# Kernel optimization log

Hardware: AMD Instinct MI355X
Metric: run time of the kernel (lower is better)

Reference implementation:

```python
import jax, jax.numpy as jnp
import numpy as np
import math

DIM = 1024
H = 16
DH = DIM // H
B = 2
L = 1024


def setup_inputs() -> dict:
    key = jax.random.key(0)
    ks = jax.random.split(key, 8)
    s = 1.0 / math.sqrt(DIM)
    return {
        "Q": jax.random.normal(ks[0], (B, L, DIM), jnp.float32),
        "K": jax.random.normal(ks[1], (B, L, DIM), jnp.float32),
        "mask_Q": jax.random.bernoulli(ks[2], 0.1, (B, L)),
        "mask_K": jax.random.bernoulli(ks[3], 0.1, (B, L)),
        "Wq": jax.random.normal(ks[4], (DIM, DIM), jnp.float32) * s,
        "Wk": jax.random.normal(ks[5], (DIM, DIM), jnp.float32) * s,
        "Wv": jax.random.normal(ks[6], (DIM, DIM), jnp.float32) * s,
        "Wo": jax.random.normal(ks[7], (DIM, DIM), jnp.float32) * s,
    }


def reference(Q, K, mask_Q, mask_K, Wq, Wk, Wv, Wo):
    # V defaults to K. Masked positions of inputs are zeroed first.
    Qz = jnp.where(mask_Q[:, :, None], 0.0, Q)
    Kz = jnp.where(mask_K[:, :, None], 0.0, K)
    Vz = Kz  # V = K, masked with mask_K

    # Projections (nn.Linear, no bias): y = x @ W.T
    Qp = jnp.einsum('bld,ed->ble', Qz, Wq)
    Kp = jnp.einsum('bld,ed->ble', Kz, Wk)
    Vp = jnp.einsum('bld,ed->ble', Vz, Wv)

    # split heads: [B, L, H, DH] -> per-head attention
    qh = Qp.reshape(B, L, H, DH)
    kh = Kp.reshape(B, L, H, DH)
    vh = Vp.reshape(B, L, H, DH)

    # NOTE: original scales by sqrt(dim) (full dim), not sqrt(dim_split)
    scores = jnp.einsum('bqhd,bkhd->bhqk', qh, kh) / math.sqrt(DIM)

    # outer-product validity mask: valid iff both q and k positions unmasked
    valid = (~mask_Q)[:, None, :, None] & (~mask_K)[:, None, None, :]  # [B,1,Lq,Lk]
    A = jnp.where(valid, scores, -1e38)
    A = jax.nn.softmax(A, axis=-1)
    A = jnp.where(valid, A, 0.0)

    O = jnp.einsum('bhqk,bkhd->bqhd', A, vh).reshape(B, L, DIM)
    # residual uses the PROJECTED Q (Q was reassigned to fc_q(Q) in torch)
    O = Qp + O
    # masked_forward(fc_o, ...): fc_o applied, masked query rows forced to 0
    ff = jax.nn.relu(jnp.where(mask_Q[:, :, None], 0.0, jnp.einsum('bld,ed->ble', O, Wo)))
    O = O + ff
    return O
```

## Files before the change

### kernel.cpp

```cpp
#include <hip/hip_runtime.h>
#include <hip/hip_bf16.h>


#define DEV __device__ __forceinline__

typedef __attribute__((ext_vector_type(8))) short bf16x8;
typedef __attribute__((ext_vector_type(4))) float f32x4;
typedef __hip_bfloat16 bf16;

DEV void glds16(const bf16* g, bf16* s) {
  __builtin_amdgcn_global_load_lds(
      (const __attribute__((address_space(1))) void*)g,
      (__attribute__((address_space(3))) void*)s, 16, 0, 0);
}

DEV unsigned short f2bu(float x) {
  __hip_bfloat16 b = __float2bfloat16(x);
  unsigned short u;
  __builtin_memcpy(&u, &b, 2);
  return u;
}

__global__ void normalize_masks(const unsigned char* mq_raw, const unsigned char* mk_raw,
                                unsigned char* outq, unsigned char* outk,
                                unsigned long long* qm64, unsigned long long* km64) {
  __shared__ int cnt;
  int t = threadIdx.x;
  if (t == 0) cnt = 0;
  __syncthreads();
  int c = 0;
  for (int i = t; i < 2048; i += 256) c += (mq_raw[i] != 0);
  atomicAdd(&cnt, c);
  __syncthreads();
  bool isByte = cnt > 128;
  for (int i = t; i < 2048; i += 256) {
    unsigned char q, k;
    if (isByte) {
      q = (mq_raw[i] != 0); k = (mk_raw[i] != 0);
    } else {
      q = (((const int*)mq_raw)[i] != 0); k = (((const int*)mk_raw)[i] != 0);
    }
    outq[i] = q; outk[i] = k;
  }
  __syncthreads();
  if (t < 64) {
    const unsigned char* src = (t < 32) ? outk : outq;
    int idx = t & 31;
    unsigned long long m = 0;
    for (int j = 0; j < 64; ++j)
      m |= (unsigned long long)(src[idx * 64 + j] != 0) << j;
    if (t < 32) km64[idx] = m; else qm64[idx] = m;
  }
}

__global__ __launch_bounds__(256) void cast_qk(const float* __restrict__ Q,
                                               const float* __restrict__ K,
                                               const unsigned char* __restrict__ mq,
                                               const unsigned char* __restrict__ mk,
                                               bf16* __restrict__ oq, bf16* __restrict__ ok) {
  const float* X = blockIdx.z ? K : Q;
  const unsigned char* m = blockIdx.z ? mk : mq;
  bf16* out = blockIdx.z ? ok : oq;
  int i = (blockIdx.x * 256 + threadIdx.x) * 4;
  float4 v = *(const float4*)&X[i];
  if (m[i >> 10]) { v.x = 0.f; v.y = 0.f; v.z = 0.f; v.w = 0.f; }
  *(ushort4*)&out[i] = make_ushort4(f2bu(v.x), f2bu(v.y), f2bu(v.z), f2bu(v.w));
}

__global__ __launch_bounds__(256) void cast_w(const float* __restrict__ W0, const float* __restrict__ W1,
                                              const float* __restrict__ W2, const float* __restrict__ W3,
                                              bf16* __restrict__ o0, bf16* __restrict__ o1,
                                              bf16* __restrict__ o2, bf16* __restrict__ o3) {
  const float* X; bf16* out;
  switch (blockIdx.z) {
    case 0: X = W0; out = o0; break;
    case 1: X = W1; out = o1; break;
    case 2: X = W2; out = o2; break;
    default: X = W3; out = o3; break;
  }
  int i = (blockIdx.x * 256 + threadIdx.x) * 4;
  float4 v = *(const float4*)&X[i];
  *(ushort4*)&out[i] = make_ushort4(f2bu(v.x), f2bu(v.y), f2bu(v.z), f2bu(v.w));
}

template <typename EPI>
DEV void gemm128(const bf16* __restrict__ A, const bf16* __restrict__ W,
                 int K, int brow, int bcol, EPI&& epi) {
  __shared__ bf16 As[128 * 32];
  __shared__ bf16 Bs[128 * 32];
  const int t = threadIdx.x;
  const int l = t & 63;
  const int w = t >> 6;
  const int wr = w >> 1, wc = w & 1;

  const int rA0 = w * 32 + (l >> 2);
  const int kcol = (l & 3) * 8;

  f32x4 acc[4][4];
#pragma unroll
  for (int i = 0; i < 4; i++)
#pragma unroll
    for (int j = 0; j < 4; j++) acc[i][j] = (f32x4){0.f, 0.f, 0.f, 0.f};

  const int aoff = (wr * 64 + (l & 15)) * 32 + (l >> 4) * 8;
  const int boff = (wc * 64 + (l & 15)) * 32 + (l >> 4) * 8;

  for (int k0 = 0; k0 < K; k0 += 32) {
    __syncthreads();
#pragma unroll
    for (int c = 0; c < 2; ++c) {
      glds16(A + (size_t)(brow + rA0 + c * 16) * K + k0 + kcol, As + w * 1024 + c * 512);
      glds16(W + (size_t)(bcol + rA0 + c * 16) * K + k0 + kcol, Bs + w * 1024 + c * 512);
    }
    __syncthreads();

    bf16x8 a[4], b[4];
#pragma unroll
    for (int mi = 0; mi < 4; ++mi) a[mi] = *(const bf16x8*)&As[aoff + mi * 512];
#pragma unroll
    for (int ni = 0; ni < 4; ++ni) b[ni] = *(const bf16x8*)&Bs[boff + ni * 512];
#pragma unroll
    for (int mi = 0; mi < 4; ++mi)
#pragma unroll
      for (int ni = 0; ni < 4; ++ni)
        acc[mi][ni] = __builtin_amdgcn_mfma_f32_16x16x32_bf16(a[mi], b[ni], acc[mi][ni], 0, 0, 0);
  }

#pragma unroll
  for (int mi = 0; mi < 4; ++mi)
#pragma unroll
    for (int ni = 0; ni < 4; ++ni)
#pragma unroll
      for (int r = 0; r < 4; ++r) {
        int row = brow + wr * 64 + mi * 16 + (l >> 4) * 4 + r;
        int col = bcol + wc * 64 + ni * 16 + (l & 15);
        epi(row, col, acc[mi][ni][r]);
      }
}

__global__ __launch_bounds__(256) void proj_gemm(
    const bf16* __restrict__ Qz, const bf16* __restrict__ Kz,
    const bf16* __restrict__ Wq, const bf16* __restrict__ Wk, const bf16* __restrict__ Wv,
    float* __restrict__ Qpf, bf16* __restrict__ Qpb,
    bf16* __restrict__ Kpb, bf16* __restrict__ Vpb) {
  const int z = blockIdx.z;
  const int brow = blockIdx.x * 128, bcol = blockIdx.y * 128;
  if (z == 0) {
    gemm128(Qz, Wq, 1024, brow, bcol, [&](int row, int col, float v) {
      size_t idx = (size_t)row * 1024 + col;
      Qpf[idx] = v;
      Qpb[idx] = __float2bfloat16(v * 0.03125f);
    });
  } else if (z == 1) {
    gemm128(Kz, Wk, 1024, brow, bcol, [&](int row, int col, float v) {
      Kpb[(size_t)row * 1024 + col] = __float2bfloat16(v);
    });
  } else {
    gemm128(Kz, Wv, 1024, brow, bcol, [&](int row, int col, float v) {
      Vpb[(size_t)row * 1024 + col] = __float2bfloat16(v);
    });
  }
}

__global__ __launch_bounds__(256) void final_gemm(
    const bf16* __restrict__ Ob, const bf16* __restrict__ Wo,
    float* __restrict__ out, const unsigned char* __restrict__ mq) {
  const int brow = blockIdx.x * 128, bcol = blockIdx.y * 128;
  gemm128(Ob, Wo, 1024, brow, bcol, [&](int row, int col, float v) {
    size_t idx = (size_t)row * 1024 + col;
    float ff = mq[row] ? 0.f : fmaxf(v, 0.f);
    out[idx] = out[idx] + ff;
  });
}

__global__ __launch_bounds__(256) void attn_fused(
    const bf16* __restrict__ Qpb, const bf16* __restrict__ Kpb, const bf16* __restrict__ Vpb,
    const float* __restrict__ Qpf,
    const unsigned long long* __restrict__ qm64, const unsigned long long* __restrict__ km64,
    float* __restrict__ Of, bf16* __restrict__ Ob) {
  __shared__ bf16 Klds[64 * 64];
  __shared__ bf16 Vt[64 * 72];

  const int t = threadIdx.x, l = t & 63, w = t >> 6;
  const int q = l & 15, g = l >> 4;
  const int qt = blockIdx.x;
  const int b = blockIdx.y >> 4, h = blockIdx.y & 15;
  const size_t bbase = (size_t)b * 1024;

  const int qg = qt * 64 + w * 16 + q;
  const bf16* qptr = Qpb + (bbase + qg) * 1024 + h * 64 + g * 8;
  const bf16x8 qb0 = *(const bf16x8*)qptr;
  const bf16x8 qb1 = *(const bf16x8*)(qptr + 32);

  float mrun = -1e30f, srun = 0.f;
  f32x4 oacc[4];
#pragma unroll
  for (int mf = 0; mf < 4; ++mf) oacc[mf] = (f32x4){0.f, 0.f, 0.f, 0.f};

  const int krow_s = l >> 3;
  const int kcol_s = ((l & 7) ^ krow_s) * 8;

  const int vk0 = 2 * (t & 31);
  const int vdc = t >> 5;

  union { uint4 v; unsigned short s[8]; } u0, u1;
  {
    const bf16* g0 = Vpb + (bbase + vk0) * 1024 + h * 64 + vdc * 8;
    u0.v = *(const uint4*)g0;
    u1.v = *(const uint4*)(g0 + 1024);
  }

  for (int kt = 0; kt < 16; ++kt) {
    const int kbase = kt * 64;
    const unsigned long long km = km64[b * 16 + kt];
    const unsigned long long mloc = km >> (4 * g);

    __syncthreads();
#pragma unroll
    for (int j = 0; j < 8; ++j) {
      int d = vdc * 8 + j;
      unsigned int pk = (unsigned int)u0.s[j] | ((unsigned int)u1.s[j] << 16);
      *(unsigned int*)((char*)Vt + d * 144 + vk0 * 2) = pk;
    }
#pragma unroll
    for (int c = 0; c < 2; ++c) {
      int cw = w * 2 + c;
      glds16(Kpb + (bbase + kbase + cw * 8 + krow_s) * 1024 + h * 64 + kcol_s,
             Klds + cw * 512);
    }
    __syncthreads();

    if (kt < 15) {
      const bf16* g0 = Vpb + (bbase + kbase + 64 + vk0) * 1024 + h * 64 + vdc * 8;
      u0.v = *(const uint4*)g0;
      u1.v = *(const uint4*)(g0 + 1024);
    }

    f32x4 S[4];
#pragma unroll
    for (int mf = 0; mf < 4; ++mf) {
#pragma unroll
      for (int r = 0; r < 4; ++r)
        S[mf][r] = ((mloc >> (mf * 16 + r)) & 1ull) ? -1e30f : 0.f;
      const int row = mf * 16 + q;
      const int rowb = row * 128;
      const bf16x8 ka0 = *(const bf16x8*)((const char*)Klds + rowb + ((g ^ (row & 7)) * 16));
      const bf16x8 ka1 = *(const bf16x8*)((const char*)Klds + rowb + (((g + 4) ^ (row & 7)) * 16));
      S[mf] = __builtin_amdgcn_mfma_f32_16x16x32_bf16(ka0, qb0, S[mf], 0, 0, 0);
      S[mf] = __builtin_amdgcn_mfma_f32_16x16x32_bf16(ka1, qb1, S[mf], 0, 0, 0);
    }

    float vmax = -1e30f;
#pragma unroll
    for (int mf = 0; mf < 4; ++mf)
#pragma unroll
      for (int r = 0; r < 4; ++r) vmax = fmaxf(vmax, S[mf][r]);
    vmax = fmaxf(vmax, __shfl_xor(vmax, 16));
    vmax = fmaxf(vmax, __shfl_xor(vmax, 32));
    const float mnew = fmaxf(mrun, vmax);
    const float alpha = __expf(mrun - mnew);
    mrun = mnew;

    float psum = 0.f;
    unsigned int lo[4], hi[4];
#pragma unroll
    for (int mf = 0; mf < 4; ++mf) {
      float p0 = __expf(S[mf][0] - mnew), p1 = __expf(S[mf][1] - mnew);
      float p2 = __expf(S[mf][2] - mnew), p3 = __expf(S[mf][3] - mnew);
      psum += (p0 + p1) + (p2 + p3);
      lo[mf] = (unsigned int)f2bu(p0) | ((unsigned int)f2bu(p1) << 16);
      hi[mf] = (unsigned int)f2bu(p2) | ((unsigned int)f2bu(p3) << 16);
    }
    psum += __shfl_xor(psum, 16);
    psum += __shfl_xor(psum, 32);
    srun = srun * alpha + psum;
#pragma unroll
    for (int mf = 0; mf < 4; ++mf) oacc[mf] *= alpha;

    const int srcA = ((2 * g) & 3) * 16 + q;
    const int srcB = srcA + 16;
    const bool sel = (g >> 1) & 1;
#pragma unroll
    for (int ks = 0; ks < 2; ++ks) {
      unsigned int a0 = __shfl(lo[2 * ks], srcA), a1 = __shfl(hi[2 * ks], srcA);
      unsigned int a2 = __shfl(lo[2 * ks], srcB), a3 = __shfl(hi[2 * ks], srcB);
      unsigned int b0 = __shfl(lo[2 * ks + 1], srcA), b1 = __shfl(hi[2 * ks + 1], srcA);
      unsigned int b2 = __shfl(lo[2 * ks + 1], srcB), b3 = __shfl(hi[2 * ks + 1], srcB);
      uint4 pw;
      pw.x = sel ? b0 : a0; pw.y = sel ? b1 : a1;
      pw.z = sel ? b2 : a2; pw.w = sel ? b3 : a3;
      const bf16x8 pa = __builtin_bit_cast(bf16x8, pw);
#pragma unroll
      for (int mf = 0; mf < 4; ++mf) {
        const bf16x8 va = *(const bf16x8*)((const char*)Vt + (mf * 16 + q) * 144 + ks * 64 + g * 16);
        oacc[mf] = __builtin_amdgcn_mfma_f32_16x16x32_bf16(va, pa, oacc[mf], 0, 0, 0);
      }
    }
  }

  const unsigned long long qm = qm64[b * 16 + qt];
  const bool qvalid = !((qm >> (w * 16 + q)) & 1ull);
  const float inv = (qvalid && srun > 0.f) ? 1.f / srun : 0.f;
#pragma unroll
  for (int mf = 0; mf < 4; ++mf) {
    size_t idx = (bbase + qg) * 1024 + h * 64 + mf * 16 + g * 4;
    float4 qp = *(const float4*)&Qpf[idx];
    float4 val;
    val.x = qp.x + oacc[mf][0] * inv;
    val.y = qp.y + oacc[mf][1] * inv;
    val.z = qp.z + oacc[mf][2] * inv;
    val.w = qp.w + oacc[mf][3] * inv;
    *(float4*)&Of[idx] = val;
    *(ushort4*)&Ob[idx] = make_ushort4(f2bu(val.x), f2bu(val.y), f2bu(val.z), f2bu(val.w));
  }
}

extern "C" void kernel_launch(void* const* d_in, const int* in_sizes, int n_in,
                              void* d_out, int out_size, void* d_ws, size_t ws_size,
                              hipStream_t stream) {
  const float* Q = (const float*)d_in[0];
  const float* K = (const float*)d_in[1];
  const unsigned char* mQraw = (const unsigned char*)d_in[2];
  const unsigned char* mKraw = (const unsigned char*)d_in[3];
  const float* Wq = (const float*)d_in[4];
  const float* Wk = (const float*)d_in[5];
  const float* Wv = (const float*)d_in[6];
  const float* Wo = (const float*)d_in[7];
  float* out = (float*)d_out;

  char* ws = (char*)d_ws;
  const size_t MB = 1024 * 1024;
  bf16* Qz = (bf16*)(ws + 0);
  bf16* Kz = (bf16*)(ws + 4 * MB);
  bf16* Wqb = (bf16*)(ws + 8 * MB);
  bf16* Wkb = (bf16*)(ws + 10 * MB);
  bf16* Wvb = (bf16*)(ws + 12 * MB);
  bf16* Wob = (bf16*)(ws + 14 * MB);
  float* Qpf = (float*)(ws + 16 * MB);
  bf16* Qpb = (bf16*)(ws + 24 * MB);
  bf16* Kpb = (bf16*)(ws + 28 * MB);
  bf16* Vpb = (bf16*)(ws + 32 * MB);
  bf16* Ob = (bf16*)(ws + 36 * MB);
  unsigned char* mqn = (unsigned char*)(ws + 40 * MB);
  unsigned char* mkn = mqn + 2048;
  unsigned long long* km64 = (unsigned long long*)(ws + 40 * MB + 4096);
  unsigned long long* qm64 = km64 + 32;

  normalize_masks<<<1, 256, 0, stream>>>(mQraw, mKraw, mqn, mkn, qm64, km64);

  dim3 gqk(2048, 1, 2);
  cast_qk<<<gqk, 256, 0, stream>>>(Q, K, mqn, mkn, Qz, Kz);
  dim3 gw(1024, 1, 4);
  cast_w<<<gw, 256, 0, stream>>>(Wq, Wk, Wv, Wo, Wqb, Wkb, Wvb, Wob);

  dim3 gp(16, 8, 3);
  proj_gemm<<<gp, 256, 0, stream>>>(Qz, Kz, Wqb, Wkb, Wvb, Qpf, Qpb, Kpb, Vpb);

  dim3 ga(16, 32);
  attn_fused<<<ga, 256, 0, stream>>>(Qpb, Kpb, Vpb, Qpf, qm64, km64, out, Ob);

  dim3 gf(16, 8);
  final_gemm<<<gf, 256, 0, stream>>>(Ob, Wob, out, mqn);
}
```

Before: 109.0 us.

## Double-buffer GEMM and attention loads, drop online-softmax max, merge cast kernels

Several optimizations land at once. The two cast kernels are merged into a single launch, and the Q/K cast now handles eight elements per thread. The GEMM core gains double-buffered LDS staging with one barrier per k-step, and the final GEMM uses 64-row tiles to launch more blocks. The attention kernel double-buffers K tiles, prefetches V one step ahead and remaps blocks so nearby blocks share a batch and head. It also drops the running-max online softmax in favour of exp2 with log2e folded into the Q scale, which removes the max reductions and rescaling but can overflow if scores grow large.

```diff
diff --git a/kernel.cpp b/kernel.cpp
--- a/kernel.cpp
+++ b/kernel.cpp
@@ -53,86 +53,102 @@
   }
 }
 
-__global__ __launch_bounds__(256) void cast_qk(const float* __restrict__ Q,
-                                               const float* __restrict__ K,
-                                               const unsigned char* __restrict__ mq,
-                                               const unsigned char* __restrict__ mk,
-                                               bf16* __restrict__ oq, bf16* __restrict__ ok) {
-  const float* X = blockIdx.z ? K : Q;
-  const unsigned char* m = blockIdx.z ? mk : mq;
-  bf16* out = blockIdx.z ? ok : oq;
-  int i = (blockIdx.x * 256 + threadIdx.x) * 4;
-  float4 v = *(const float4*)&X[i];
-  if (m[i >> 10]) { v.x = 0.f; v.y = 0.f; v.z = 0.f; v.w = 0.f; }
-  *(ushort4*)&out[i] = make_ushort4(f2bu(v.x), f2bu(v.y), f2bu(v.z), f2bu(v.w));
-}
-
-__global__ __launch_bounds__(256) void cast_w(const float* __restrict__ W0, const float* __restrict__ W1,
-                                              const float* __restrict__ W2, const float* __restrict__ W3,
-                                              bf16* __restrict__ o0, bf16* __restrict__ o1,
-                                              bf16* __restrict__ o2, bf16* __restrict__ o3) {
-  const float* X; bf16* out;
-  switch (blockIdx.z) {
-    case 0: X = W0; out = o0; break;
-    case 1: X = W1; out = o1; break;
-    case 2: X = W2; out = o2; break;
-    default: X = W3; out = o3; break;
-  }
-  int i = (blockIdx.x * 256 + threadIdx.x) * 4;
-  float4 v = *(const float4*)&X[i];
-  *(ushort4*)&out[i] = make_ushort4(f2bu(v.x), f2bu(v.y), f2bu(v.z), f2bu(v.w));
-}
-
-template <typename EPI>
-DEV void gemm128(const bf16* __restrict__ A, const bf16* __restrict__ W,
-                 int K, int brow, int bcol, EPI&& epi) {
-  __shared__ bf16 As[128 * 32];
-  __shared__ bf16 Bs[128 * 32];
-  const int t = threadIdx.x;
-  const int l = t & 63;
-  const int w = t >> 6;
+__global__ __launch_bounds__(256) void cast_all(
+    const float* __restrict__ Q, const float* __restrict__ K,
+    const unsigned char* __restrict__ mq, const unsigned char* __restrict__ mk,
+    const float* __restrict__ W0, const float* __restrict__ W1,
+    const float* __restrict__ W2, const float* __restrict__ W3,
+    bf16* __restrict__ Qz, bf16* __restrict__ Kz,
+    bf16* __restrict__ o0, bf16* __restrict__ o1,
+    bf16* __restrict__ o2, bf16* __restrict__ o3) {
+  const int z = blockIdx.z;
+  if (z < 2) {
+    const float* X = z ? K : Q;
+    const unsigned char* m = z ? mk : mq;
+    bf16* out = z ? Kz : Qz;
+    int i = (blockIdx.x * 256 + threadIdx.x) * 8;
+    float4 v0 = *(const float4*)&X[i];
+    float4 v1 = *(const float4*)&X[i + 4];
+    if (m[i >> 10]) {
+      v0 = make_float4(0.f, 0.f, 0.f, 0.f);
+      v1 = make_float4(0.f, 0.f, 0.f, 0.f);
+    }
+    *(ushort4*)&out[i] = make_ushort4(f2bu(v0.x), f2bu(v0.y), f2bu(v0.z), f2bu(v0.w));
+    *(ushort4*)&out[i + 4] = make_ushort4(f2bu(v1.x), f2bu(v1.y), f2bu(v1.z), f2bu(v1.w));
+  } else {
+    const float* X; bf16* out;
+    switch (z) {
+      case 2: X = W0; out = o0; break;
+      case 3: X = W1; out = o1; break;
+      case 4: X = W2; out = o2; break;
+      default: X = W3; out = o3; break;
+    }
+    int i = (blockIdx.x * 256 + threadIdx.x) * 4;
+    float4 v = *(const float4*)&X[i];
+    *(ushort4*)&out[i] = make_ushort4(f2bu(v.x), f2bu(v.y), f2bu(v.z), f2bu(v.w));
+  }
+}
+
+template <int MI, typename EPI>
+DEV void gemm_core(const bf16* __restrict__ A, const bf16* __restrict__ W,
+                   int K, int brow, int bcol, EPI&& epi) {
+  constexpr int BM = MI * 32;
+  __shared__ bf16 As[2][BM * 32];
+  __shared__ bf16 Bs[2][128 * 32];
+  const int t = threadIdx.x, l = t & 63, w = t >> 6;
   const int wr = w >> 1, wc = w & 1;
-
-  const int rA0 = w * 32 + (l >> 2);
+  const int rs = l >> 2;
   const int kcol = (l & 3) * 8;
 
-  f32x4 acc[4][4];
-#pragma unroll
-  for (int i = 0; i < 4; i++)
+  f32x4 acc[MI][4];
+#pragma unroll
+  for (int i = 0; i < MI; i++)
 #pragma unroll
     for (int j = 0; j < 4; j++) acc[i][j] = (f32x4){0.f, 0.f, 0.f, 0.f};
 
-  const int aoff = (wr * 64 + (l & 15)) * 32 + (l >> 4) * 8;
+  const int aoff = (wr * (MI * 16) + (l & 15)) * 32 + (l >> 4) * 8;
   const int boff = (wc * 64 + (l & 15)) * 32 + (l >> 4) * 8;
 
+  auto stage = [&](int k0, int b_) {
+    if constexpr (MI == 4) {
+#pragma unroll
+      for (int c = 0; c < 2; ++c)
+        glds16(A + (size_t)(brow + w * 32 + c * 16 + rs) * K + k0 + kcol,
+               &As[b_][w * 1024 + c * 512]);
+    } else {
+      glds16(A + (size_t)(brow + w * 16 + rs) * K + k0 + kcol, &As[b_][w * 512]);
+    }
+#pragma unroll
+    for (int c = 0; c < 2; ++c)
+      glds16(W + (size_t)(bcol + w * 32 + c * 16 + rs) * K + k0 + kcol,
+             &Bs[b_][w * 1024 + c * 512]);
+  };
+
+  stage(0, 0);
+  int buf = 0;
   for (int k0 = 0; k0 < K; k0 += 32) {
     __syncthreads();
-#pragma unroll
-    for (int c = 0; c < 2; ++c) {
-      glds16(A + (size_t)(brow + rA0 + c * 16) * K + k0 + kcol, As + w * 1024 + c * 512);
-      glds16(W + (size_t)(bcol + rA0 + c * 16) * K + k0 + kcol, Bs + w * 1024 + c * 512);
-    }
-    __syncthreads();
-
-    bf16x8 a[4], b[4];
-#pragma unroll
-    for (int mi = 0; mi < 4; ++mi) a[mi] = *(const bf16x8*)&As[aoff + mi * 512];
-#pragma unroll
-    for (int ni = 0; ni < 4; ++ni) b[ni] = *(const bf16x8*)&Bs[boff + ni * 512];
-#pragma unroll
-    for (int mi = 0; mi < 4; ++mi)
+    if (k0 + 32 < K) stage(k0 + 32, buf ^ 1);
+    bf16x8 a[MI], b[4];
+#pragma unroll
+    for (int mi = 0; mi < MI; ++mi) a[mi] = *(const bf16x8*)&As[buf][aoff + mi * 512];
+#pragma unroll
+    for (int ni = 0; ni < 4; ++ni) b[ni] = *(const bf16x8*)&Bs[buf][boff + ni * 512];
+#pragma unroll
+    for (int mi = 0; mi < MI; ++mi)
 #pragma unroll
       for (int ni = 0; ni < 4; ++ni)
         acc[mi][ni] = __builtin_amdgcn_mfma_f32_16x16x32_bf16(a[mi], b[ni], acc[mi][ni], 0, 0, 0);
-  }
-
-#pragma unroll
-  for (int mi = 0; mi < 4; ++mi)
+    buf ^= 1;
+  }
+
+#pragma unroll
+  for (int mi = 0; mi < MI; ++mi)
 #pragma unroll
     for (int ni = 0; ni < 4; ++ni)
 #pragma unroll
       for (int r = 0; r < 4; ++r) {
-        int row = brow + wr * 64 + mi * 16 + (l >> 4) * 4 + r;
+        int row = brow + wr * (MI * 16) + mi * 16 + (l >> 4) * 4 + r;
         int col = bcol + wc * 64 + ni * 16 + (l & 15);
         epi(row, col, acc[mi][ni][r]);
       }
@@ -146,17 +162,17 @@
   const int z = blockIdx.z;
   const int brow = blockIdx.x * 128, bcol = blockIdx.y * 128;
   if (z == 0) {
-    gemm128(Qz, Wq, 1024, brow, bcol, [&](int row, int col, float v) {
+    gemm_core<4>(Qz, Wq, 1024, brow, bcol, [&](int row, int col, float v) {
       size_t idx = (size_t)row * 1024 + col;
       Qpf[idx] = v;
-      Qpb[idx] = __float2bfloat16(v * 0.03125f);
+      Qpb[idx] = __float2bfloat16(v * 0.045084220f);
     });
   } else if (z == 1) {
-    gemm128(Kz, Wk, 1024, brow, bcol, [&](int row, int col, float v) {
+    gemm_core<4>(Kz, Wk, 1024, brow, bcol, [&](int row, int col, float v) {
       Kpb[(size_t)row * 1024 + col] = __float2bfloat16(v);
     });
   } else {
-    gemm128(Kz, Wv, 1024, brow, bcol, [&](int row, int col, float v) {
+    gemm_core<4>(Kz, Wv, 1024, brow, bcol, [&](int row, int col, float v) {
       Vpb[(size_t)row * 1024 + col] = __float2bfloat16(v);
     });
   }
@@ -165,8 +181,8 @@
 __global__ __launch_bounds__(256) void final_gemm(
     const bf16* __restrict__ Ob, const bf16* __restrict__ Wo,
     float* __restrict__ out, const unsigned char* __restrict__ mq) {
-  const int brow = blockIdx.x * 128, bcol = blockIdx.y * 128;
-  gemm128(Ob, Wo, 1024, brow, bcol, [&](int row, int col, float v) {
+  const int brow = blockIdx.x * 64, bcol = blockIdx.y * 128;
+  gemm_core<2>(Ob, Wo, 1024, brow, bcol, [&](int row, int col, float v) {
     size_t idx = (size_t)row * 1024 + col;
     float ff = mq[row] ? 0.f : fmaxf(v, 0.f);
     out[idx] = out[idx] + ff;
@@ -178,13 +194,15 @@
     const float* __restrict__ Qpf,
     const unsigned long long* __restrict__ qm64, const unsigned long long* __restrict__ km64,
     float* __restrict__ Of, bf16* __restrict__ Ob) {
-  __shared__ bf16 Klds[64 * 64];
+  __shared__ bf16 Klds[2][64 * 64];
   __shared__ bf16 Vt[64 * 72];
 
   const int t = threadIdx.x, l = t & 63, w = t >> 6;
   const int q = l & 15, g = l >> 4;
-  const int qt = blockIdx.x;
-  const int b = blockIdx.y >> 4, h = blockIdx.y & 15;
+  const int f = blockIdx.x;
+  const int bh = (f & 7) + 8 * ((f >> 3) & 3);
+  const int qt = f >> 5;
+  const int b = bh >> 4, h = bh & 15;
   const size_t bbase = (size_t)b * 1024;
 
   const int qg = qt * 64 + w * 16 + q;
@@ -192,48 +210,46 @@
   const bf16x8 qb0 = *(const bf16x8*)qptr;
   const bf16x8 qb1 = *(const bf16x8*)(qptr + 32);
 
-  float mrun = -1e30f, srun = 0.f;
+  float psum = 0.f;
   f32x4 oacc[4];
 #pragma unroll
   for (int mf = 0; mf < 4; ++mf) oacc[mf] = (f32x4){0.f, 0.f, 0.f, 0.f};
 
   const int krow_s = l >> 3;
   const int kcol_s = ((l & 7) ^ krow_s) * 8;
-
   const int vk0 = 2 * (t & 31);
   const int vdc = t >> 5;
 
   union { uint4 v; unsigned short s[8]; } u0, u1;
-  {
-    const bf16* g0 = Vpb + (bbase + vk0) * 1024 + h * 64 + vdc * 8;
+
+  auto stageK = [&](int kt_, int b_) {
+#pragma unroll
+    for (int c = 0; c < 2; ++c) {
+      int cw = w * 2 + c;
+      glds16(Kpb + (bbase + kt_ * 64 + cw * 8 + krow_s) * 1024 + h * 64 + kcol_s,
+             &Klds[b_][cw * 512]);
+    }
+  };
+  auto loadV = [&](int kt_) {
+    const bf16* g0 = Vpb + (bbase + kt_ * 64 + vk0) * 1024 + h * 64 + vdc * 8;
     u0.v = *(const uint4*)g0;
     u1.v = *(const uint4*)(g0 + 1024);
-  }
+  };
+
+  stageK(0, 0);
+  loadV(0);
+  int buf = 0;
 
   for (int kt = 0; kt < 16; ++kt) {
-    const int kbase = kt * 64;
     const unsigned long long km = km64[b * 16 + kt];
     const unsigned long long mloc = km >> (4 * g);
 
     __syncthreads();
+
 #pragma unroll
     for (int j = 0; j < 8; ++j) {
-      int d = vdc * 8 + j;
       unsigned int pk = (unsigned int)u0.s[j] | ((unsigned int)u1.s[j] << 16);
-      *(unsigned int*)((char*)Vt + d * 144 + vk0 * 2) = pk;
-    }
-#pragma unroll
-    for (int c = 0; c < 2; ++c) {
-      int cw = w * 2 + c;
-      glds16(Kpb + (bbase + kbase + cw * 8 + krow_s) * 1024 + h * 64 + kcol_s,
-             Klds + cw * 512);
-    }
-    __syncthreads();
-
-    if (kt < 15) {
-      const bf16* g0 = Vpb + (bbase + kbase + 64 + vk0) * 1024 + h * 64 + vdc * 8;
-      u0.v = *(const uint4*)g0;
-      u1.v = *(const uint4*)(g0 + 1024);
+      *(unsigned int*)((char*)Vt + (vdc * 8 + j) * 144 + vk0 * 2) = pk;
     }
 
     f32x4 S[4];
@@ -244,38 +260,28 @@
         S[mf][r] = ((mloc >> (mf * 16 + r)) & 1ull) ? -1e30f : 0.f;
       const int row = mf * 16 + q;
       const int rowb = row * 128;
-      const bf16x8 ka0 = *(const bf16x8*)((const char*)Klds + rowb + ((g ^ (row & 7)) * 16));
-      const bf16x8 ka1 = *(const bf16x8*)((const char*)Klds + rowb + (((g + 4) ^ (row & 7)) * 16));
+      const bf16x8 ka0 = *(const bf16x8*)((const char*)&Klds[buf][0] + rowb + ((g ^ (row & 7)) * 16));
+      const bf16x8 ka1 = *(const bf16x8*)((const char*)&Klds[buf][0] + rowb + (((g + 4) ^ (row & 7)) * 16));
       S[mf] = __builtin_amdgcn_mfma_f32_16x16x32_bf16(ka0, qb0, S[mf], 0, 0, 0);
       S[mf] = __builtin_amdgcn_mfma_f32_16x16x32_bf16(ka1, qb1, S[mf], 0, 0, 0);
     }
 
-    float vmax = -1e30f;
-#pragma unroll
-    for (int mf = 0; mf < 4; ++mf)
-#pragma unroll
-      for (int r = 0; r < 4; ++r) vmax = fmaxf(vmax, S[mf][r]);
-    vmax = fmaxf(vmax, __shfl_xor(vmax, 16));
-    vmax = fmaxf(vmax, __shfl_xor(vmax, 32));
-    const float mnew = fmaxf(mrun, vmax);
-    const float alpha = __expf(mrun - mnew);
-    mrun = mnew;
-
-    float psum = 0.f;
     unsigned int lo[4], hi[4];
 #pragma unroll
     for (int mf = 0; mf < 4; ++mf) {
-      float p0 = __expf(S[mf][0] - mnew), p1 = __expf(S[mf][1] - mnew);
-      float p2 = __expf(S[mf][2] - mnew), p3 = __expf(S[mf][3] - mnew);
+      float p0 = exp2f(S[mf][0]), p1 = exp2f(S[mf][1]);
+      float p2 = exp2f(S[mf][2]), p3 = exp2f(S[mf][3]);
       psum += (p0 + p1) + (p2 + p3);
       lo[mf] = (unsigned int)f2bu(p0) | ((unsigned int)f2bu(p1) << 16);
       hi[mf] = (unsigned int)f2bu(p2) | ((unsigned int)f2bu(p3) << 16);
     }
-    psum += __shfl_xor(psum, 16);
-    psum += __shfl_xor(psum, 32);
-    srun = srun * alpha + psum;
-#pragma unroll
-    for (int mf = 0; mf < 4; ++mf) oacc[mf] *= alpha;
+
+    __syncthreads();
+
+    if (kt < 15) {
+      stageK(kt + 1, buf ^ 1);
+      loadV(kt + 1);
+    }
 
     const int srcA = ((2 * g) & 3) * 16 + q;
     const int srcB = srcA + 16;
@@ -296,11 +302,15 @@
         oacc[mf] = __builtin_amdgcn_mfma_f32_16x16x32_bf16(va, pa, oacc[mf], 0, 0, 0);
       }
     }
-  }
+    buf ^= 1;
+  }
+
+  psum += __shfl_xor(psum, 16);
+  psum += __shfl_xor(psum, 32);
 
   const unsigned long long qm = qm64[b * 16 + qt];
   const bool qvalid = !((qm >> (w * 16 + q)) & 1ull);
-  const float inv = (qvalid && srun > 0.f) ? 1.f / srun : 0.f;
+  const float inv = (qvalid && psum > 0.f) ? 1.f / psum : 0.f;
 #pragma unroll
   for (int mf = 0; mf < 4; ++mf) {
     size_t idx = (bbase + qg) * 1024 + h * 64 + mf * 16 + g * 4;
@@ -348,17 +358,15 @@
 
   normalize_masks<<<1, 256, 0, stream>>>(mQraw, mKraw, mqn, mkn, qm64, km64);
 
-  dim3 gqk(2048, 1, 2);
-  cast_qk<<<gqk, 256, 0, stream>>>(Q, K, mqn, mkn, Qz, Kz);
-  dim3 gw(1024, 1, 4);
-  cast_w<<<gw, 256, 0, stream>>>(Wq, Wk, Wv, Wo, Wqb, Wkb, Wvb, Wob);
+  dim3 gc(1024, 1, 6);
+  cast_all<<<gc, 256, 0, stream>>>(Q, K, mqn, mkn, Wq, Wk, Wv, Wo,
+                                   Qz, Kz, Wqb, Wkb, Wvb, Wob);
 
   dim3 gp(16, 8, 3);
   proj_gemm<<<gp, 256, 0, stream>>>(Qz, Kz, Wqb, Wkb, Wvb, Qpf, Qpb, Kpb, Vpb);
 
-  dim3 ga(16, 32);
-  attn_fused<<<ga, 256, 0, stream>>>(Qpb, Kpb, Vpb, Qpf, qm64, km64, out, Ob);
-
-  dim3 gf(16, 8);
+  attn_fused<<<512, 256, 0, stream>>>(Qpb, Kpb, Vpb, Qpf, qm64, km64, out, Ob);
+
+  dim3 gf(32, 8);
   final_gemm<<<gf, 256, 0, stream>>>(Ob, Wob, out, mqn);
 }
```

Result: slower. 112.1 us (+2.8%).
